# Optimization experiments

Measured on AMD Instinct MI355X. Metric: run time of the kernel, lower is better.

Reference implementation:

```python
import jax, jax.numpy as jnp
import numpy as np

K = 3  # spline order
G = 5  # grid_size

def bspline(x):
    # Cox-de Boor B-spline basis over uniform grid on [-1,1] extended by K knots each side.
    h = 2.0 / G
    grid = jnp.arange(-K, G + K + 1, dtype=x.dtype) * h - 1.0  # [G+2K+1]
    xe = x[..., None]
    b = ((xe >= grid[:-1]) & (xe < grid[1:])).astype(x.dtype)  # order-0 bases [..., G+2K]
    for p in range(1, K + 1):
        b = ((xe - grid[:-(p + 1)]) / (grid[p:-1] - grid[:-(p + 1)]) * b[..., :-1]
             + (grid[p + 1:] - xe) / (grid[p + 1:] - grid[1:-p]) * b[..., 1:])
    return b  # [..., G+K]

def kan_conv(x, wb, ws, k):
    # x: [B,Cin,H,W] -> patches [B, Cin*k*k, H', W'] -> KANLinear per spatial position
    p = jax.lax.conv_general_dilated_patches(x, (k, k), (1, 1), 'VALID')
    p = jnp.moveaxis(p, 1, -1)  # [B,H',W',F]
    base = jax.nn.silu(p) @ wb.T
    spline = jnp.einsum('bhwig,oig->bhwo', bspline(p), ws)
    return jnp.moveaxis(base + spline, -1, 1)  # [B,Cout,H',W']

def maxpool2(x):
    return jax.lax.reduce_window(x, -jnp.inf, jax.lax.max, (1, 1, 2, 2), (1, 1, 2, 2), 'VALID')

def setup_inputs() -> dict:
    key = jax.random.key(0)
    ks = jax.random.split(key, 9)
    B = 4096
    s = 0.1
    return {
        'x': jax.random.normal(ks[0], (B, 1, 28, 28), jnp.float32),
        'wb1': jax.random.normal(ks[1], (5, 9), jnp.float32) * s,
        'ws1': jax.random.normal(ks[2], (5, 9, G + K), jnp.float32) * s,
        'wb2': jax.random.normal(ks[3], (5, 125), jnp.float32) * s,
        'ws2': jax.random.normal(ks[4], (5, 125, G + K), jnp.float32) * s,
        'wb3': jax.random.normal(ks[5], (2, 45), jnp.float32) * s,
        'ws3': jax.random.normal(ks[6], (2, 45, G + K), jnp.float32) * s,
        'fc_w': jax.random.normal(ks[7], (200, 98), jnp.float32) * s,
        'fc_b': jnp.zeros((200,), jnp.float32),
    }

def reference(x, wb1, ws1, wb2, ws2, wb3, ws3, fc_w, fc_b):
    h = kan_conv(x, wb1, ws1, 3)    # [B,5,26,26]
    h = maxpool2(h)                 # [B,5,13,13]
    h = kan_conv(h, wb2, ws2, 5)    # [B,5,9,9]
    h = kan_conv(h, wb3, ws3, 3)    # [B,2,7,7]
    h = h.reshape(h.shape[0], -1)   # [B,98]
    return h @ fc_w.T + fc_b        # [B,200]
```

## Files before the change

### kernel.cpp

```cpp
#include <hip/hip_runtime.h>


typedef _Float16 h2 __attribute__((ext_vector_type(2)));
typedef _Float16 f16x8 __attribute__((ext_vector_type(8)));
typedef float f32x4 __attribute__((ext_vector_type(4)));
typedef unsigned int uint_t;
typedef unsigned long long u64;

__device__ __forceinline__ uint_t pk(float a, float b) {
    h2 v; v[0] = (_Float16)a; v[1] = (_Float16)b;
    union { h2 h; uint_t u; } c; c.h = v; return c.u;
}

__device__ __forceinline__ float silu_f(float v) {
    return v / (1.0f + __expf(-v));
}

struct RecW { u64 R0, R1; uint_t R2; };
__device__ __forceinline__ RecW rec_words(float v) {
    float s  = silu_f(v);
    float t  = (v + 2.2f) * 2.5f;
    float cf = floorf(t);
    int   c  = (int)cf;
    float u  = t - cf;
    float u2 = u * u, u3 = u2 * u;
    float w  = 1.0f - u;
    const float k6 = 0.16666667f;
    float n0 = k6 * u3;
    float n1 = k6 * (-3.0f * u3 + 3.0f * u2 + 3.0f * u + 1.0f);
    float n2 = k6 * (3.0f * u3 - 6.0f * u2 + 4.0f);
    float n3 = k6 * (w * w * w);
    u64 H = ((u64)pk(n1, n0) << 32) | (u64)pk(n3, n2);
    if ((unsigned)c > 10u) H = 0;
    int cc = c < 0 ? 0 : (c > 10 ? 10 : c);
    int L  = cc * 16 - 48;
    u64 sl_lo = (L < 64) ? (H << (L & 63)) : 0;
    u64 hi_a  = (L == 0) ? 0 : (H >> ((64 - L) & 63));
    u64 hi_b  = H << ((L - 64) & 63);
    u64 sl_hi = (L < 64) ? hi_a : hi_b;
    u64 sr    = H >> ((-L) & 63);
    u64 B0 = (L >= 0) ? sl_lo : sr;
    u64 B1 = (L >= 0) ? sl_hi : 0;
    RecW r;
    r.R0 = (B0 << 16) | (u64)pk(s, 0.0f);
    r.R1 = (B0 >> 48) | (B1 << 16);
    r.R2 = (uint_t)(B1 >> 48);
    return r;
}

__device__ __forceinline__ void write_rec16s(_Float16* p, int off, float v) {
    RecW rw = rec_words(v);
    uint4 lo, hi;
    lo.x = (uint_t)rw.R0; lo.y = (uint_t)(rw.R0 >> 32);
    lo.z = (uint_t)rw.R1; lo.w = (uint_t)(rw.R1 >> 32);
    hi.x = rw.R2; hi.y = 0; hi.z = 0; hi.w = 0;
    *(uint4*)(p + off)       = lo;
    *(uint4*)(p + (8 ^ off)) = hi;
}

__device__ __forceinline__ void write_rec10(_Float16* p, float v) {
    RecW rw = rec_words(v);
    uint_t* d = (uint_t*)p;
    d[0] = (uint_t)rw.R0; d[1] = (uint_t)(rw.R0 >> 32);
    d[2] = (uint_t)rw.R1; d[3] = (uint_t)(rw.R1 >> 32);
    d[4] = rw.R2;
}

#define FCWT_BYTE_OFF   0
#define W1COL_BYTE_OFF  78400
#define W2COL_BYTE_OFF  80320
#define W3COL_BYTE_OFF  99520

__global__ __launch_bounds__(256) void kan_prep(
    const float* __restrict__ wb1, const float* __restrict__ ws1,
    const float* __restrict__ wb2, const float* __restrict__ ws2,
    const float* __restrict__ wb3, const float* __restrict__ ws3,
    const float* __restrict__ fcw, float* __restrict__ fcwT,
    _Float16* __restrict__ w1col, _Float16* __restrict__ w2col,
    _Float16* __restrict__ w3col)
{
    int gtid = blockIdx.x * 256 + threadIdx.x;
    int gstr = gridDim.x * 256;
    for (int i = gtid; i < 19600; i += gstr) {
        int o = i / 98, j = i % 98;
        fcwT[j * 200 + o] = fcw[i];
    }
    for (int i = gtid; i < 960; i += gstr) {
        int n = i / 160, k = i % 160;
        int rec = k >> 4, f = k & 15;
        float v = 0.f;
        if (n < 5 && rec < 9 && f < 9)
            v = (f == 0) ? wb1[n * 9 + rec] : ws1[(n * 9 + rec) * 8 + (f - 1)];
        w1col[i] = (_Float16)v;
    }
    for (int i = gtid; i < 9600; i += gstr) {
        int n = i / 1600, k2 = i % 1600;
        int tap = k2 >> 6, k = k2 & 63;
        int di = tap / 5, dj = tap % 5;
        int c = k / 10, f = k % 10;
        float v = 0.f;
        if (n < 5 && k < 50 && f < 9) {
            int r = n * 125 + c * 25 + di * 5 + dj;
            v = (f == 0) ? wb2[r] : ws2[r * 8 + (f - 1)];
        }
        w2col[i] = (_Float16)v;
    }
    for (int i = gtid; i < 3456; i += gstr) {
        int n = i / 576, k2 = i % 576;
        int tap = k2 >> 6, k = k2 & 63;
        int di = tap / 3, dj = tap % 3;
        int c = k / 10, f = k % 10;
        float v = 0.f;
        if (n < 2 && k < 50 && f < 9) {
            int r = n * 45 + c * 9 + di * 3 + dj;
            v = (f == 0) ? wb3[r] : ws3[r * 8 + (f - 1)];
        }
        w3col[i] = (_Float16)v;
    }
}

__global__ __launch_bounds__(256) void kan_fused(
    const float* __restrict__ x,
    const _Float16* __restrict__ w1col,
    const _Float16* __restrict__ w2col,
    const _Float16* __restrict__ w3col,
    const float* __restrict__ fcwT,
    const float* __restrict__ fcb,
    float* __restrict__ out)
{
    __shared__ __align__(16) _Float16 smemA[12544];
    __shared__ __align__(16) float    smemB[408];
    float* buf = smemB;
    float* h3f = smemB;

    const int b   = blockIdx.x;
    const int tid = threadIdx.x;
    const int wv  = __builtin_amdgcn_readfirstlane(tid >> 6);
    const int ln  = tid & 63;

    const int m   = ln & 15;
    const int kb  = ln >> 4;
    const int hr  = kb >> 1;
    const int s8  = (kb & 1) * 8;
    const int nn  = m < 5 ? m : 5;

#pragma unroll
    for (int i = tid; i < 408; i += 256) smemB[i] = 0.f;
#pragma unroll 1
    for (int i = tid; i < 784; i += 256)
        write_rec16s(&smemA[i * 16], (i & 4) << 1, x[b * 784 + i]);
    __syncthreads();

    {
        f16x8 Bf[5];
#pragma unroll
        for (int ks = 0; ks < 5; ++ks)
            Bf[ks] = *(const f16x8*)(w1col + nn * 160 + ks * 32 + kb * 8);
        const int dpix[10] = {0, 1, 2, 28, 29, 30, 56, 57, 58, 0};
#pragma unroll 1
        for (int tile = wv; tile < 43; tile += 4) {
            int p = tile * 16 + m; p = p > 675 ? 675 : p;
            int pix0 = (p / 26) * 28 + (p % 26);
            f32x4 acc = {0.f, 0.f, 0.f, 0.f};
#pragma unroll
            for (int ks = 0; ks < 5; ++ks) {
                int dp = hr ? dpix[2 * ks + 1] : dpix[2 * ks];
                int p2 = pix0 + dp;
                int addr = p2 * 16 + (s8 ^ ((p2 & 4) << 1));
                f16x8 av = *(const f16x8*)(smemA + addr);
                acc = __builtin_amdgcn_mfma_f32_16x16x32_f16(av, Bf[ks], acc, 0, 0, 0);
            }
            int srow = tile * 16 + kb * 4;
#pragma unroll
            for (int r = 0; r < 4; ++r) {
                int s = srow + r;
                if (m < 5 && s < 676)
                    smemA[s * 16 + (8 ^ ((s & 4) << 1)) + 2 + m] = (_Float16)acc[r];
            }
        }
    }
    __syncthreads();

    float mx0, mx1, mx2, mx3 = 0.f;
    {
        auto pool = [&](int i) -> float {
            int pp = i / 5, c = i % 5;
            int ph = pp / 13, pw = pp % 13;
            int s0 = ph * 52 + pw * 2;
            int s1 = s0 + 1, s2 = s0 + 26, s3 = s0 + 27;
            float v00 = (float)smemA[s0 * 16 + (8 ^ ((s0 & 4) << 1)) + 2 + c];
            float v01 = (float)smemA[s1 * 16 + (8 ^ ((s1 & 4) << 1)) + 2 + c];
            float v10 = (float)smemA[s2 * 16 + (8 ^ ((s2 & 4) << 1)) + 2 + c];
            float v11 = (float)smemA[s3 * 16 + (8 ^ ((s3 & 4) << 1)) + 2 + c];
            return fmaxf(fmaxf(v00, v01), fmaxf(v10, v11));
        };
        mx0 = pool(tid);
        mx1 = pool(tid + 256);
        mx2 = pool(tid + 512);
        if (tid < 77) mx3 = pool(tid + 768);
    }
    __syncthreads();

    {
        auto st = [&](int i, float v) {
            int pp = i / 5, c = i % 5;
            write_rec10(&smemA[pp * 72 + c * 10], v);
        };
        st(tid, mx0);
        st(tid + 256, mx1);
        st(tid + 512, mx2);
        if (tid < 77) st(tid + 768, mx3);
    }
    __syncthreads();

    {
        int ryb[6];
#pragma unroll
        for (int t = 0; t < 6; ++t) {
            int p = t * 16 + m; p = p > 80 ? 80 : p;
            ryb[t] = (p / 9) * 13 + (p % 9);
        }
        f32x4 acc[6];
#pragma unroll
        for (int t = 0; t < 6; ++t) { f32x4 z = {0.f,0.f,0.f,0.f}; acc[t] = z; }
#pragma unroll 1
        for (int tap = wv; tap < 25; tap += 4) {
            int di = tap / 5, dj = tap % 5;
            const _Float16* wrow = w2col + nn * 1600 + tap * 64 + kb * 8;
            f16x8 bv0 = *(const f16x8*)(wrow);
            f16x8 bv1 = *(const f16x8*)(wrow + 32);
            int qoff = di * 13 + dj;
#pragma unroll
            for (int t = 0; t < 6; ++t) {
                const _Float16* ab = smemA + (ryb[t] + qoff) * 72 + kb * 8;
                acc[t] = __builtin_amdgcn_mfma_f32_16x16x32_f16(
                             *(const f16x8*)(ab), bv0, acc[t], 0, 0, 0);
                acc[t] = __builtin_amdgcn_mfma_f32_16x16x32_f16(
                             *(const f16x8*)(ab + 32), bv1, acc[t], 0, 0, 0);
            }
        }
        int prow = kb * 4;
#pragma unroll
        for (int t = 0; t < 6; ++t) {
#pragma unroll
            for (int r = 0; r < 4; ++r) {
                int pp = t * 16 + prow + r;
                if (m < 5 && pp < 81) atomicAdd(&buf[m * 81 + pp], acc[t][r]);
            }
        }
    }
    __syncthreads();

#pragma unroll 1
    for (int i = tid; i < 405; i += 256) {
        int pp = i / 5, o = i % 5;
        write_rec10(&smemA[pp * 72 + o * 10], buf[o * 81 + pp]);
    }
    __syncthreads();

    {
        int p3 = wv * 16 + m; p3 = p3 > 48 ? 48 : p3;
        int ry3 = (p3 / 7) * 9 + (p3 % 7);
        f32x4 acc = {0.f, 0.f, 0.f, 0.f};
#pragma unroll 1
        for (int tap = 0; tap < 9; ++tap) {
            int di = tap / 3, dj = tap % 3;
            const _Float16* wrow = w3col + nn * 576 + tap * 64 + kb * 8;
            f16x8 bv0 = *(const f16x8*)(wrow);
            f16x8 bv1 = *(const f16x8*)(wrow + 32);
            const _Float16* ab = smemA + (ry3 + di * 9 + dj) * 72 + kb * 8;
            acc = __builtin_amdgcn_mfma_f32_16x16x32_f16(*(const f16x8*)(ab),      bv0, acc, 0, 0, 0);
            acc = __builtin_amdgcn_mfma_f32_16x16x32_f16(*(const f16x8*)(ab + 32), bv1, acc, 0, 0, 0);
        }
#pragma unroll
        for (int r = 0; r < 4; ++r) {
            int pout = wv * 16 + kb * 4 + r;
            if (m < 2 && pout < 49) h3f[m * 49 + pout] = acc[r];
        }
    }
    __syncthreads();

    if (tid < 200) {
        float a0 = 0.f, a1 = 0.f;
#pragma unroll 7
        for (int j = 0; j < 98; j += 2) {
            a0 += fcwT[j * 200 + tid]       * h3f[j];
            a1 += fcwT[(j + 1) * 200 + tid] * h3f[j + 1];
        }
        out[b * 200 + tid] = fcb[tid] + a0 + a1;
    }
}

extern "C" void kernel_launch(void* const* d_in, const int* in_sizes, int n_in,
                              void* d_out, int out_size, void* d_ws, size_t ws_size,
                              hipStream_t stream) {
    const float* x   = (const float*)d_in[0];
    const float* wb1 = (const float*)d_in[1];
    const float* ws1 = (const float*)d_in[2];
    const float* wb2 = (const float*)d_in[3];
    const float* ws2 = (const float*)d_in[4];
    const float* wb3 = (const float*)d_in[5];
    const float* ws3 = (const float*)d_in[6];
    const float* fcw = (const float*)d_in[7];
    const float* fcb = (const float*)d_in[8];
    float* out = (float*)d_out;

    float*    fcwT  = (float*)((char*)d_ws + FCWT_BYTE_OFF);
    _Float16* w1col = (_Float16*)((char*)d_ws + W1COL_BYTE_OFF);
    _Float16* w2col = (_Float16*)((char*)d_ws + W2COL_BYTE_OFF);
    _Float16* w3col = (_Float16*)((char*)d_ws + W3COL_BYTE_OFF);

    kan_prep<<<32, 256, 0, stream>>>(wb1, ws1, wb2, ws2, wb3, ws3, fcw,
                                     fcwT, w1col, w2col, w3col);

    int B = in_sizes[0] / 784;
    kan_fused<<<B, 256, 0, stream>>>(x, w1col, w2col, w3col, fcwT, fcb, out);
}
```

Before: 172.9 us.

## Replace LDS atomics with per-wave partials and merge maxpool into one pass

Conv1 outputs are written to a dense channel-major fp16 buffer in a separate shared array, so maxpool reads packed pairs and writes the layer-2 records directly. This removes one barrier and the register staging of pooled values. The layer-2 cross-wave reduction now stores per-wave partial sums into a larger shared buffer that are summed afterwards, instead of doing shared-memory atomicAdd, so the zero-init is no longer needed. Shared memory use grows by about 5 KB per block, which may affect occupancy.

```diff
diff --git a/kernel.cpp b/kernel.cpp
--- a/kernel.cpp
+++ b/kernel.cpp
@@ -7,6 +7,7 @@
 typedef unsigned int uint_t;
 typedef unsigned long long u64;
 
+__device__ __forceinline__ h2 as_h2(uint_t u) { union { uint_t u; h2 h; } c; c.u = u; return c.h; }
 __device__ __forceinline__ uint_t pk(float a, float b) {
     h2 v; v[0] = (_Float16)a; v[1] = (_Float16)b;
     union { h2 h; uint_t u; } c; c.h = v; return c.u;
@@ -129,9 +130,10 @@
     float* __restrict__ out)
 {
     __shared__ __align__(16) _Float16 smemA[12544];
-    __shared__ __align__(16) float    smemB[408];
-    float* buf = smemB;
-    float* h3f = smemB;
+    __shared__ __align__(16) float    smemB[1696];
+    _Float16* P2h   = (_Float16*)smemB;
+    float*    part2 = smemB;
+    float*    h3f   = smemB;
 
     const int b   = blockIdx.x;
     const int tid = threadIdx.x;
@@ -144,8 +146,6 @@
     const int s8  = (kb & 1) * 8;
     const int nn  = m < 5 ? m : 5;
 
-#pragma unroll
-    for (int i = tid; i < 408; i += 256) smemB[i] = 0.f;
 #pragma unroll 1
     for (int i = tid; i < 784; i += 256)
         write_rec16s(&smemA[i * 16], (i & 4) << 1, x[b * 784 + i]);
@@ -174,42 +174,22 @@
 #pragma unroll
             for (int r = 0; r < 4; ++r) {
                 int s = srow + r;
-                if (m < 5 && s < 676)
-                    smemA[s * 16 + (8 ^ ((s & 4) << 1)) + 2 + m] = (_Float16)acc[r];
+                if (m < 5 && s < 676) P2h[m * 676 + s] = (_Float16)acc[r];
             }
         }
     }
     __syncthreads();
 
-    float mx0, mx1, mx2, mx3 = 0.f;
-    {
-        auto pool = [&](int i) -> float {
-            int pp = i / 5, c = i % 5;
-            int ph = pp / 13, pw = pp % 13;
-            int s0 = ph * 52 + pw * 2;
-            int s1 = s0 + 1, s2 = s0 + 26, s3 = s0 + 27;
-            float v00 = (float)smemA[s0 * 16 + (8 ^ ((s0 & 4) << 1)) + 2 + c];
-            float v01 = (float)smemA[s1 * 16 + (8 ^ ((s1 & 4) << 1)) + 2 + c];
-            float v10 = (float)smemA[s2 * 16 + (8 ^ ((s2 & 4) << 1)) + 2 + c];
-            float v11 = (float)smemA[s3 * 16 + (8 ^ ((s3 & 4) << 1)) + 2 + c];
-            return fmaxf(fmaxf(v00, v01), fmaxf(v10, v11));
-        };
-        mx0 = pool(tid);
-        mx1 = pool(tid + 256);
-        mx2 = pool(tid + 512);
-        if (tid < 77) mx3 = pool(tid + 768);
-    }
-    __syncthreads();
-
-    {
-        auto st = [&](int i, float v) {
-            int pp = i / 5, c = i % 5;
-            write_rec10(&smemA[pp * 72 + c * 10], v);
-        };
-        st(tid, mx0);
-        st(tid + 256, mx1);
-        st(tid + 512, mx2);
-        if (tid < 77) st(tid + 768, mx3);
+#pragma unroll 1
+    for (int i = tid; i < 845; i += 256) {
+        int c = i / 169, pp = i % 169;
+        int ph = pp / 13, pw = pp % 13;
+        const _Float16* q = P2h + c * 676 + (2 * ph) * 26 + 2 * pw;
+        h2 a = as_h2(*(const uint_t*)q);
+        h2 d = as_h2(*(const uint_t*)(q + 26));
+        float mx = fmaxf(fmaxf((float)a[0], (float)a[1]),
+                         fmaxf((float)d[0], (float)d[1]));
+        write_rec10(&smemA[pp * 72 + c * 10], mx);
     }
     __syncthreads();
 
@@ -245,7 +225,7 @@
 #pragma unroll
             for (int r = 0; r < 4; ++r) {
                 int pp = t * 16 + prow + r;
-                if (m < 5 && pp < 81) atomicAdd(&buf[m * 81 + pp], acc[t][r]);
+                if (m < 5 && pp < 81) part2[(wv * 5 + m) * 81 + pp] = acc[t][r];
             }
         }
     }
@@ -253,8 +233,10 @@
 
 #pragma unroll 1
     for (int i = tid; i < 405; i += 256) {
-        int pp = i / 5, o = i % 5;
-        write_rec10(&smemA[pp * 72 + o * 10], buf[o * 81 + pp]);
+        int o = i / 81, pp = i % 81;
+        float v = part2[(0 * 5 + o) * 81 + pp] + part2[(1 * 5 + o) * 81 + pp]
+                + part2[(2 * 5 + o) * 81 + pp] + part2[(3 * 5 + o) * 81 + pp];
+        write_rec10(&smemA[pp * 72 + o * 10], v);
     }
     __syncthreads();
 
```

Measured after the change: 146.1 us. -15.5%, faster.
